# Optimization experiments

Hardware: AMD Instinct MI355X
Metric: run time of the kernel (lower is better)

Reference implementation:

```python
import jax, jax.numpy as jnp
import numpy as np

D_MODEL = 1024
N_HEADS = 16
HEAD_DIM = D_MODEL // N_HEADS
ROPE_THETA = 10000.0


def _apply_rope(t, pos):
    # t: [B, H, S, hd]; pos: [B, S] int. Half-split (NeoX-style) rotation.
    hd = t.shape[-1]
    inv_freq = 1.0 / (ROPE_THETA ** (jnp.arange(0, hd, 2, dtype=t.dtype) / hd))  # [hd/2]
    ang = pos.astype(t.dtype)[:, None, :, None] * inv_freq  # [B, 1, S, hd/2]
    cos, sin = jnp.cos(ang), jnp.sin(ang)
    t1, t2 = t[..., 0::2], t[..., 1::2]
    r1 = t1 * cos - t2 * sin
    r2 = t1 * sin + t2 * cos
    # interleave back
    return jnp.stack([r1, r2], axis=-1).reshape(t.shape)


def setup_inputs() -> dict:
    key = jax.random.key(0)
    k1, k2, k3 = jax.random.split(key, 3)
    B, S = 4, 2048
    x = jax.random.normal(k1, (B, S, D_MODEL), dtype=jnp.float32)
    positions = jnp.broadcast_to(jnp.arange(S, dtype=jnp.int32), (B, S))
    Wqkv = jax.random.normal(k2, (3 * D_MODEL, D_MODEL), dtype=jnp.float32) * (1.0 / np.sqrt(D_MODEL))
    bqkv = jnp.zeros((3 * D_MODEL,), dtype=jnp.float32)
    Wo = jax.random.normal(k3, (D_MODEL, D_MODEL), dtype=jnp.float32) * (1.0 / np.sqrt(D_MODEL))
    bo = jnp.zeros((D_MODEL,), dtype=jnp.float32)
    return {"x": x, "positions": positions, "Wqkv": Wqkv, "bqkv": bqkv, "Wo": Wo, "bo": bo}


def reference(x, positions, Wqkv, bqkv, Wo, bo):
    B, S, D = x.shape
    # fused QKV projection (torch Linear: x @ W^T + b)
    qkv = x @ Wqkv.T + bqkv                      # [B, S, 3D]
    q, k, v = jnp.split(qkv, 3, axis=-1)
    def to_heads(t):
        return t.reshape(B, S, N_HEADS, HEAD_DIM).transpose(0, 2, 1, 3)  # [B, H, S, hd]
    q, k, v = to_heads(q), to_heads(k), to_heads(v)
    q = _apply_rope(q, positions)
    k = _apply_rope(k, positions)
    scale = 1.0 / np.sqrt(HEAD_DIM)
    scores = jnp.einsum('bhqd,bhkd->bhqk', q, k) * scale   # [B, H, S, S]
    causal = jnp.tril(jnp.ones((S, S), dtype=bool))
    scores = jnp.where(causal, scores, jnp.finfo(scores.dtype).min)
    attn = jax.nn.softmax(scores, axis=-1)
    h = jnp.einsum('bhqk,bhkd->bhqd', attn, v)             # [B, H, S, hd]
    h = h.transpose(0, 2, 1, 3).reshape(B, S, D)
    return h @ Wo.T + bo
```

## Files before the change

kernel.cpp:

```cpp
#include <hip/hip_runtime.h>

#define DEV static __device__ __forceinline__

typedef __attribute__((ext_vector_type(8))) short short8;
typedef __attribute__((ext_vector_type(4))) short short4v;
typedef __attribute__((ext_vector_type(4))) float f32x4;
typedef __attribute__((ext_vector_type(4))) unsigned short ushort4v;
typedef __attribute__((ext_vector_type(4))) float float4v;

#define DM 1024
#define NH 16
#define HD 64
#define SS 2048
#define TOK 8192

DEV unsigned short f2bf(float f) {
  union { float f; unsigned u; } v; v.f = f;
  unsigned r = v.u + 0x7FFFu + ((v.u >> 16) & 1u);
  return (unsigned short)(r >> 16);
}
DEV float bf2f(unsigned short h) {
  union { unsigned u; float f; } v; v.u = ((unsigned)h) << 16;
  return v.f;
}

#define MFMA16x32(a, b, c) __builtin_amdgcn_mfma_f32_16x16x32_bf16((a), (b), (c), 0, 0, 0)

DEV f32x4 mfma_pv(short4v a, short4v b, f32x4 c) {
#if __has_builtin(__builtin_amdgcn_mfma_f32_16x16x16bf16_1k)
  return __builtin_amdgcn_mfma_f32_16x16x16bf16_1k(a, b, c, 0, 0, 0);
#else
  f32x4 d;
  asm("v_mfma_f32_16x16x16_bf16 %0, %1, %2, %3" : "=&v"(d) : "v"(a), "v"(b), "v"(c));
  return d;
#endif
}

DEV void gload_lds16(const unsigned short* g, unsigned short* l) {
  __builtin_amdgcn_global_load_lds(
      (const __attribute__((address_space(1))) void*)g,
      (__attribute__((address_space(3))) void*)l, 16, 0, 0);
}

__global__ __launch_bounds__(256) void k_cvt(const float* __restrict__ in,
                                             unsigned short* __restrict__ out, int n4) {
  int i = blockIdx.x * 256 + threadIdx.x;
  if (i >= n4) return;
  float4v v = ((const float4v*)in)[i];
  ushort4v o;
  o[0] = f2bf(v[0]); o[1] = f2bf(v[1]); o[2] = f2bf(v[2]); o[3] = f2bf(v[3]);
  ((ushort4v*)out)[i] = o;
}

__global__ __launch_bounds__(256) void k_tab(const int* __restrict__ pos,
                                             float* __restrict__ tc, float* __restrict__ ts) {
  int i = blockIdx.x * 256 + threadIdx.x;
  int t = i >> 5, fi = i & 31;
  float p = (float)pos[t];
  float inv = powf(10000.0f, -(float)fi / 32.0f);
  float a = p * inv;
  float sv, cv;
  sincosf(a, &sv, &cv);
  tc[i] = cv;
  ts[i] = sv;
}

__global__ __launch_bounds__(256) void k_rope(unsigned short* __restrict__ Q,
                                              unsigned short* __restrict__ K,
                                              const float* __restrict__ tc,
                                              const float* __restrict__ ts) {
  int idx = blockIdx.x * 256 + threadIdx.x;
  int bh = idx >> 11, s = idx & 2047, b = bh >> 4;
  const float* tcp = tc + ((size_t)(b * SS + s)) * 32;
  const float* tsp = ts + ((size_t)(b * SS + s)) * 32;
  size_t base = (size_t)idx * 64;
  for (int which = 0; which < 2; ++which) {
    unsigned short* P = which ? K : Q;
    short8* rp = (short8*)(P + base);
#pragma unroll
    for (int ch = 0; ch < 8; ++ch) {
      short8 v = rp[ch];
      short8 r;
#pragma unroll
      for (int p = 0; p < 4; ++p) {
        int pi = ch * 4 + p;
        float e = bf2f((unsigned short)v[2 * p]);
        float o = bf2f((unsigned short)v[2 * p + 1]);
        float c = tcp[pi], sn = tsp[pi];
        r[2 * p]     = (short)f2bf(e * c - o * sn);
        r[2 * p + 1] = (short)f2bf(e * sn + o * c);
      }
      rp[ch] = r;
    }
  }
}

template <int MODE>
__global__ __launch_bounds__(256) void k_gemm_bt(
    const unsigned short* __restrict__ A, const unsigned short* __restrict__ Bm,
    const float* __restrict__ bias, void* __restrict__ out0, void* __restrict__ out1,
    void* __restrict__ out2, int M, int N, int K) {
  __shared__ __align__(16) unsigned short As[128 * 64];
  __shared__ __align__(16) unsigned short Bs[128 * 64];
  int wid = threadIdx.x >> 6, lane = threadIdx.x & 63;
  int l16 = lane & 15, lq = lane >> 4;
  int m0 = blockIdx.y * 128, n0 = blockIdx.x * 128;
  int wr = wid >> 1, wc = wid & 1;

  f32x4 acc[4][4];
#pragma unroll
  for (int i = 0; i < 4; i++)
#pragma unroll
    for (int j = 0; j < 4; j++) acc[i][j] = (f32x4){0.f, 0.f, 0.f, 0.f};

  int c0 = wid * 4;
  int srow = lane >> 3;
  int skcol = (lane & 7) * 8;
  int nkt = K >> 6;
  for (int kt = 0; kt < nkt; ++kt) {
    int k0 = kt << 6;
    __syncthreads();
#pragma unroll
    for (int i = 0; i < 4; ++i) {
      int c = c0 + i;
      const unsigned short* sa = A + (size_t)(m0 + c * 8 + srow) * K + (k0 + skcol);
      gload_lds16(sa, &As[c * 512]);
      const unsigned short* sb = Bm + (size_t)(n0 + c * 8 + srow) * K + (k0 + skcol);
      gload_lds16(sb, &Bs[c * 512]);
    }
    __syncthreads();
#pragma unroll
    for (int kk = 0; kk < 2; ++kk) {
      int ko = kk * 32 + lq * 8;
      short8 af[4], bfr[4];
#pragma unroll
      for (int mi = 0; mi < 4; ++mi)
        af[mi] = *(const short8*)&As[(wr * 64 + mi * 16 + l16) * 64 + ko];
#pragma unroll
      for (int ni = 0; ni < 4; ++ni)
        bfr[ni] = *(const short8*)&Bs[(wc * 64 + ni * 16 + l16) * 64 + ko];
#pragma unroll
      for (int mi = 0; mi < 4; ++mi)
#pragma unroll
        for (int ni = 0; ni < 4; ++ni)
          acc[mi][ni] = MFMA16x32(af[mi], bfr[ni], acc[mi][ni]);
    }
  }

  if (MODE == 0) {
    float* C = (float*)out0;
#pragma unroll
    for (int mi = 0; mi < 4; ++mi) {
      int row = m0 + wr * 64 + mi * 16 + lq * 4;
#pragma unroll
      for (int ni = 0; ni < 4; ++ni) {
        int col = n0 + wc * 64 + ni * 16 + l16;
        float bv = bias[col];
#pragma unroll
        for (int j = 0; j < 4; ++j)
          C[(size_t)(row + j) * N + col] = acc[mi][ni][j] + bv;
      }
    }
  } else {
    unsigned short* Qb = (unsigned short*)out0;
    unsigned short* Kb = (unsigned short*)out1;
    unsigned short* Vt = (unsigned short*)out2;
#pragma unroll
    for (int mi = 0; mi < 4; ++mi) {
      int row = m0 + wr * 64 + mi * 16 + lq * 4;
      int b = row >> 11, s = row & 2047;
#pragma unroll
      for (int ni = 0; ni < 4; ++ni) {
        int col = n0 + wc * 64 + ni * 16 + l16;
        int sel = col >> 10;
        int hh = (col >> 6) & 15;
        int d = col & 63;
        float bv = bias[col];
        if (sel < 2) {
          unsigned short* P = sel ? Kb : Qb;
          size_t p = ((size_t)(b * NH + hh) * SS + s) * 64 + d;
#pragma unroll
          for (int j = 0; j < 4; ++j)
            P[p + (size_t)j * 64] = f2bf(acc[mi][ni][j] + bv);
        } else {
          size_t p = ((size_t)(b * NH + hh) * 64 + d) * SS + s;
          ushort4v o;
#pragma unroll
          for (int j = 0; j < 4; ++j) o[j] = f2bf(acc[mi][ni][j] + bv);
          *(ushort4v*)&Vt[p] = o;
        }
      }
    }
  }
}

__global__ __launch_bounds__(256) void k_attn(const unsigned short* __restrict__ Q,
                                              const unsigned short* __restrict__ K,
                                              const unsigned short* __restrict__ Vt,
                                              unsigned short* __restrict__ H) {
  __shared__ __align__(16) unsigned short Kbuf[2 * 4096];
  __shared__ __align__(16) unsigned short Vbuf[2 * 4096];

  int lin = blockIdx.x;
  int bh = lin & 63;
  int p = lin >> 6;
  int b = bh >> 4, h = bh & 15;
  int wid = threadIdx.x >> 6, lane = threadIdx.x & 63;
  int l16 = lane & 15, lq = lane >> 4;
  int sx = l16 & 7;
  const unsigned short* Qh = Q + (size_t)bh * SS * 64;
  const unsigned short* Kh = K + (size_t)bh * SS * 64;
  const unsigned short* Vh = Vt + (size_t)bh * 64 * SS;

  for (int seg = 0; seg < 2; ++seg) {
    int g = seg ? (31 - p) : p;
    int qbase = g * 64 + wid * 16;
    int qrow = qbase + l16;
    int ntk = g + 1;

    short8 aq[2];
    {
      const unsigned short* qp = Qh + (size_t)qrow * 64 + lq * 8;
      aq[0] = *(const short8*)qp;
      aq[1] = *(const short8*)(qp + 32);
    }
    f32x4 o[4];
#pragma unroll
    for (int i = 0; i < 4; ++i) o[i] = (f32x4){0.f, 0.f, 0.f, 0.f};
    float lsum = 0.f;

#pragma unroll
    for (int i = 0; i < 2; ++i) {
      int c = threadIdx.x + (i << 8);
      int row = c >> 3, col = ((c & 7) ^ (row & 7)) << 3;
      gload_lds16(Kh + (size_t)row * 64 + col, &Kbuf[c * 8]);
      gload_lds16(Vh + (size_t)row * SS + col, &Vbuf[c * 8]);
    }
    __syncthreads();

    int cur = 0;
    for (int kt = 0; kt < ntk; ++kt) {
      if (kt + 1 < ntk) {
        int kb1 = (kt + 1) << 6;
        int nb_ = (cur ^ 1) * 4096;
#pragma unroll
        for (int i = 0; i < 2; ++i) {
          int c = threadIdx.x + (i << 8);
          int row = c >> 3, col = ((c & 7) ^ (row & 7)) << 3;
          gload_lds16(Kh + (size_t)(kb1 + row) * 64 + col, &Kbuf[nb_ + c * 8]);
          gload_lds16(Vh + (size_t)row * SS + kb1 + col, &Vbuf[nb_ + c * 8]);
        }
      }
      int kb = kt << 6;
      const unsigned short* Kb_ = &Kbuf[cur * 4096];
      const unsigned short* Vb_ = &Vbuf[cur * 4096];

      f32x4 sacc[4];
#pragma unroll
      for (int nb = 0; nb < 4; ++nb) {
        int r = nb * 16 + l16;
        short8 bk0 = *(const short8*)&Kb_[r * 64 + ((lq ^ sx) << 3)];
        short8 bk1 = *(const short8*)&Kb_[r * 64 + (((4 | lq) ^ sx) << 3)];
        f32x4 z = (f32x4){0.f, 0.f, 0.f, 0.f};
        z = MFMA16x32(bk0, aq[0], z);
        z = MFMA16x32(bk1, aq[1], z);
        sacc[nb] = z;
      }
      float sc[4][4];
#pragma unroll
      for (int nb = 0; nb < 4; ++nb)
#pragma unroll
        for (int j = 0; j < 4; ++j) sc[nb][j] = sacc[nb][j] * 0.18033688f;
      if (kt == g) {
#pragma unroll
        for (int nb = 0; nb < 4; ++nb)
#pragma unroll
          for (int j = 0; j < 4; ++j) {
            int key = kb + nb * 16 + lq * 4 + j;
            if (key > qrow) sc[nb][j] = -1e30f;
          }
      }
      short4v pa[4];
#pragma unroll
      for (int nb = 0; nb < 4; ++nb) {
        float pv[4];
#pragma unroll
        for (int j = 0; j < 4; ++j) {
          float e;
          asm("v_exp_f32 %0, %1" : "=v"(e) : "v"(sc[nb][j]));
          lsum += e;
          pv[j] = e;
        }
        union { unsigned u[2]; short4v s4; } pk;
        asm("v_cvt_pk_bf16_f32 %0, %1, %2" : "=v"(pk.u[0]) : "v"(pv[0]), "v"(pv[1]));
        asm("v_cvt_pk_bf16_f32 %0, %1, %2" : "=v"(pk.u[1]) : "v"(pv[2]), "v"(pv[3]));
        pa[nb] = pk.s4;
      }
#pragma unroll
      for (int ni = 0; ni < 4; ++ni) {
        int row = ni * 16 + l16;
        f32x4 acc = o[ni];
#pragma unroll
        for (int nb = 0; nb < 4; ++nb) {
          int ch = (2 * nb + (lq >> 1)) ^ sx;
          short4v bv = *(const short4v*)&Vb_[row * 64 + ch * 8 + ((lq & 1) << 2)];
          acc = mfma_pv(pa[nb], bv, acc);
        }
        o[ni] = acc;
      }
      __syncthreads();
      cur ^= 1;
    }

    float red = lsum;
    red += __shfl_xor(red, 16, 64);
    red += __shfl_xor(red, 32, 64);
    float inv[4];
#pragma unroll
    for (int j = 0; j < 4; ++j) {
      int src = (lane & 48) + ((lane >> 4) & 3) * 4 + j;
      inv[j] = 1.0f / __shfl(red, src, 64);
    }
#pragma unroll
    for (int ni = 0; ni < 4; ++ni) {
      int d = h * 64 + ni * 16 + l16;
#pragma unroll
      for (int j = 0; j < 4; ++j) {
        int s = qbase + lq * 4 + j;
        H[((size_t)(b * SS + s)) * 1024 + d] = f2bf(o[ni][j] * inv[j]);
      }
    }
  }
}

extern "C" void kernel_launch(void* const* d_in, const int* in_sizes, int n_in,
                              void* d_out, int out_size, void* d_ws, size_t ws_size,
                              hipStream_t stream) {
  const float* x    = (const float*)d_in[0];
  const int*   pos  = (const int*)d_in[1];
  const float* Wqkv = (const float*)d_in[2];
  const float* bqkv = (const float*)d_in[3];
  const float* Wo   = (const float*)d_in[4];
  const float* bo   = (const float*)d_in[5];
  float* out = (float*)d_out;

  char* w = (char*)d_ws;
  unsigned short* x_bf    = (unsigned short*)(w + 0);
  unsigned short* h_bf    = x_bf;
  unsigned short* wqkv_bf = (unsigned short*)(w + 16777216);
  unsigned short* wo_bf   = (unsigned short*)(w + 23068672);
  unsigned short* Qb      = (unsigned short*)(w + 25165824);
  unsigned short* Kb      = (unsigned short*)(w + 41943040);
  unsigned short* Vt      = (unsigned short*)(w + 58720256);
  float* tabc             = (float*)(w + 75497472);
  float* tabs             = (float*)(w + 76546048);

  k_cvt<<<8192, 256, 0, stream>>>(x, x_bf, 2097152);
  k_cvt<<<3072, 256, 0, stream>>>(Wqkv, wqkv_bf, 786432);
  k_cvt<<<1024, 256, 0, stream>>>(Wo, wo_bf, 262144);
  k_tab<<<1024, 256, 0, stream>>>(pos, tabc, tabs);
  k_gemm_bt<1><<<dim3(24, 64), 256, 0, stream>>>(x_bf, wqkv_bf, bqkv, Qb, Kb, Vt, TOK, 3072, DM);
  k_rope<<<512, 256, 0, stream>>>(Qb, Kb, tabc, tabs);
  k_attn<<<1024, 256, 0, stream>>>(Qb, Kb, Vt, h_bf);
  k_gemm_bt<0><<<dim3(8, 64), 256, 0, stream>>>(h_bf, wo_bf, bo, out, nullptr, nullptr, TOK, DM, DM);
}
```

Baseline: 221.4 us.

## Triple-buffer GEMM LDS pipeline with 256x128 tiles and XOR-swizzled shared memory

Replaces the single-buffered bf16 GEMM, which synchronised twice per k-step, with a triple-buffered pipeline. Global-to-LDS loads for tile t+2 are issued while tile t is being computed, with vmcnt waits and one barrier per step. The block tile grows to 256x128 with 8 waves. LDS columns are XOR-swizzled to cut bank conflicts on the fragment reads. About 144KB of LDS limits occupancy to one block per CU, and the launch grid shrinks to match.

```diff
diff --git a/kernel.cpp b/kernel.cpp
--- a/kernel.cpp
+++ b/kernel.cpp
@@ -96,16 +96,39 @@
 }
 
 template <int MODE>
-__global__ __launch_bounds__(256) void k_gemm_bt(
+__global__ __launch_bounds__(512) void k_gemm3(
     const unsigned short* __restrict__ A, const unsigned short* __restrict__ Bm,
     const float* __restrict__ bias, void* __restrict__ out0, void* __restrict__ out1,
     void* __restrict__ out2, int M, int N, int K) {
-  __shared__ __align__(16) unsigned short As[128 * 64];
-  __shared__ __align__(16) unsigned short Bs[128 * 64];
-  int wid = threadIdx.x >> 6, lane = threadIdx.x & 63;
-  int l16 = lane & 15, lq = lane >> 4;
-  int m0 = blockIdx.y * 128, n0 = blockIdx.x * 128;
-  int wr = wid >> 1, wc = wid & 1;
+  __shared__ __align__(16) unsigned short Abuf[3][256 * 64];
+  __shared__ __align__(16) unsigned short Bbuf[3][128 * 64];
+  const int tid = threadIdx.x;
+  const int wid = tid >> 6, lane = tid & 63;
+  const int l16 = lane & 15, lq = lane >> 4;
+  const int wr = wid >> 1, wc = wid & 1;
+  const int m0 = blockIdx.y * 256, n0 = blockIdx.x * 128;
+  const int r8 = lane >> 3, c8 = lane & 7;
+  const int NT = K >> 6;
+  const int sx = l16 & 7;
+
+#define STAGE_G3(T, BSEL)                                                           \
+  {                                                                                 \
+    int k0_ = (T) << 6;                                                             \
+    unsigned short* ab_ = Abuf[BSEL];                                               \
+    unsigned short* bb_ = Bbuf[BSEL];                                               \
+    _Pragma("unroll")                                                               \
+    for (int i_ = 0; i_ < 4; ++i_) {                                                \
+      int o_ = wid * 4 + i_;                                                        \
+      gload_lds16(A + (size_t)(m0 + o_ * 8 + r8) * K + k0_ + ((c8 ^ r8) << 3),      \
+                  &ab_[o_ * 512]);                                                  \
+    }                                                                               \
+    _Pragma("unroll")                                                               \
+    for (int i_ = 0; i_ < 2; ++i_) {                                                \
+      int o_ = wid * 2 + i_;                                                        \
+      gload_lds16(Bm + (size_t)(n0 + o_ * 8 + r8) * K + k0_ + ((c8 ^ r8) << 3),     \
+                  &bb_[o_ * 512]);                                                  \
+    }                                                                               \
+  }
 
   f32x4 acc[4][4];
 #pragma unroll
@@ -113,39 +136,46 @@
 #pragma unroll
     for (int j = 0; j < 4; j++) acc[i][j] = (f32x4){0.f, 0.f, 0.f, 0.f};
 
-  int c0 = wid * 4;
-  int srow = lane >> 3;
-  int skcol = (lane & 7) * 8;
-  int nkt = K >> 6;
-  for (int kt = 0; kt < nkt; ++kt) {
-    int k0 = kt << 6;
-    __syncthreads();
-#pragma unroll
-    for (int i = 0; i < 4; ++i) {
-      int c = c0 + i;
-      const unsigned short* sa = A + (size_t)(m0 + c * 8 + srow) * K + (k0 + skcol);
-      gload_lds16(sa, &As[c * 512]);
-      const unsigned short* sb = Bm + (size_t)(n0 + c * 8 + srow) * K + (k0 + skcol);
-      gload_lds16(sb, &Bs[c * 512]);
-    }
-    __syncthreads();
+  STAGE_G3(0, 0)
+  STAGE_G3(1, 1)
+  asm volatile("s_waitcnt vmcnt(6)" ::: "memory");
+  __builtin_amdgcn_s_barrier();
+  __builtin_amdgcn_sched_barrier(0);
+
+  int cb = 0, sb = 2;
+  for (int t = 0; t < NT; ++t) {
+    if (t + 2 < NT) STAGE_G3(t + 2, sb)
+    const unsigned short* Ab = Abuf[cb];
+    const unsigned short* Bb = Bbuf[cb];
 #pragma unroll
     for (int kk = 0; kk < 2; ++kk) {
-      int ko = kk * 32 + lq * 8;
+      int sw0 = ((kk * 4 + lq) ^ sx) << 3;
       short8 af[4], bfr[4];
 #pragma unroll
       for (int mi = 0; mi < 4; ++mi)
-        af[mi] = *(const short8*)&As[(wr * 64 + mi * 16 + l16) * 64 + ko];
+        af[mi] = *(const short8*)&Ab[(wr * 64 + mi * 16 + l16) * 64 + sw0];
 #pragma unroll
       for (int ni = 0; ni < 4; ++ni)
-        bfr[ni] = *(const short8*)&Bs[(wc * 64 + ni * 16 + l16) * 64 + ko];
+        bfr[ni] = *(const short8*)&Bb[(wc * 64 + ni * 16 + l16) * 64 + sw0];
 #pragma unroll
       for (int mi = 0; mi < 4; ++mi)
 #pragma unroll
         for (int ni = 0; ni < 4; ++ni)
           acc[mi][ni] = MFMA16x32(af[mi], bfr[ni], acc[mi][ni]);
     }
-  }
+    if (t + 1 < NT) {
+      if (t + 3 <= NT) {
+        asm volatile("s_waitcnt vmcnt(6)" ::: "memory");
+      } else {
+        asm volatile("s_waitcnt vmcnt(0)" ::: "memory");
+      }
+      __builtin_amdgcn_s_barrier();
+      __builtin_amdgcn_sched_barrier(0);
+    }
+    cb = (cb == 2) ? 0 : cb + 1;
+    sb = (sb == 2) ? 0 : sb + 1;
+  }
+#undef STAGE_G3
 
   if (MODE == 0) {
     float* C = (float*)out0;
@@ -359,8 +389,8 @@
   k_cvt<<<3072, 256, 0, stream>>>(Wqkv, wqkv_bf, 786432);
   k_cvt<<<1024, 256, 0, stream>>>(Wo, wo_bf, 262144);
   k_tab<<<1024, 256, 0, stream>>>(pos, tabc, tabs);
-  k_gemm_bt<1><<<dim3(24, 64), 256, 0, stream>>>(x_bf, wqkv_bf, bqkv, Qb, Kb, Vt, TOK, 3072, DM);
+  k_gemm3<1><<<dim3(24, 32), 512, 0, stream>>>(x_bf, wqkv_bf, bqkv, Qb, Kb, Vt, TOK, 3072, DM);
   k_rope<<<512, 256, 0, stream>>>(Qb, Kb, tabc, tabs);
   k_attn<<<1024, 256, 0, stream>>>(Qb, Kb, Vt, h_bf);
-  k_gemm_bt<0><<<dim3(8, 64), 256, 0, stream>>>(h_bf, wo_bf, bo, out, nullptr, nullptr, TOK, DM, DM);
-}
+  k_gemm3<0><<<dim3(8, 32), 512, 0, stream>>>(h_bf, wo_bf, bo, out, nullptr, nullptr, TOK, DM, DM);
+}
```

Result: faster. 214.9 us (-2.9%).
